# Kernel optimization log

Hardware: AMD Instinct MI355X
Metric: run time of the kernel (lower is better)

## Reference

```python
import jax, jax.numpy as jnp
import numpy as np

N_NODES = 50000
N_EDGES = 800000
IN_F, H_F, OUT_F = 512, 128, 64


def _graph_conv(x, W, b, src, dst, norm_src, norm_dst):
    # DGL GraphConv, norm='both': out = D_dst^-1/2 * A * (D_src^-1/2 * x) @ W + b
    # weight applied before aggregation (in_feats >= out_feats path) — math identical.
    h = (x * norm_src[:, None]) @ W                      # [N, out_f]
    agg = jax.ops.segment_sum(h[src], dst, num_segments=N_NODES)  # SpMM gather/scatter
    return agg * norm_dst[:, None] + b


def setup_inputs() -> dict:
    key = jax.random.key(0)
    ks = jax.random.split(key, 12)
    x = jax.random.normal(ks[0], (N_NODES, IN_F), dtype=jnp.float32)
    src = jax.random.randint(ks[1], (N_EDGES,), 0, N_NODES, dtype=jnp.int64)
    dst = jax.random.randint(ks[2], (N_EDGES,), 0, N_NODES, dtype=jnp.int64)

    def glorot(k, fan_in, fan_out):
        s = jnp.sqrt(6.0 / (fan_in + fan_out)).astype(jnp.float32)
        return jax.random.uniform(k, (fan_in, fan_out), jnp.float32, -s, s)

    return {
        'x': x, 'src': src, 'dst': dst,
        'W1': glorot(ks[3], IN_F, H_F), 'b1': jnp.zeros((H_F,), jnp.float32),
        'W2': glorot(ks[4], H_F, H_F), 'b2': jnp.zeros((H_F,), jnp.float32),
        'W3': glorot(ks[5], H_F, H_F), 'b3': jnp.zeros((H_F,), jnp.float32),
        'W4': glorot(ks[6], H_F, OUT_F), 'b4': jnp.zeros((OUT_F,), jnp.float32),
        'embedding_layer': 3,
    }


def reference(x, src, dst, W1, b1, W2, b2, W3, b3, W4, b4, embedding_layer):
    ones = jnp.ones((N_EDGES,), jnp.float32)
    out_deg = jnp.maximum(jax.ops.segment_sum(ones, src, num_segments=N_NODES), 1.0)
    in_deg = jnp.maximum(jax.ops.segment_sum(ones, dst, num_segments=N_NODES), 1.0)
    norm_src = jax.lax.rsqrt(out_deg)
    norm_dst = jax.lax.rsqrt(in_deg)

    h1 = jax.nn.relu(_graph_conv(x, W1, b1, src, dst, norm_src, norm_dst))
    h2 = jax.nn.relu(_graph_conv(h1, W2, b2, src, dst, norm_src, norm_dst))
    h3 = jax.nn.relu(_graph_conv(h2, W3, b3, src, dst, norm_src, norm_dst))
    h4 = _graph_conv(h3, W4, b4, src, dst, norm_src, norm_dst)

    hidden = [h1, h2, h3, h4][embedding_layer - 1]  # embedding_layer is a static int
    return (h4, hidden, x)
```

## Files before the change

### kernel.cpp

```cpp
#include <hip/hip_runtime.h>

#define N_NODES 50000
#define N_EDGES 800000
#define IN_F 512
#define H_F 128
#define OUT_F 64


__global__ void detect_kernel(const void* __restrict__ edges, int* __restrict__ flag) {
    if (threadIdx.x == 0 && blockIdx.x == 0) {
        const long long* p = (const long long*)edges;
        int is64 = 1;
        for (int k = 0; k < 256; k++) {
            long long v = p[k];
            if (v < 0 || v >= N_NODES) { is64 = 0; break; }
        }
        flag[0] = is64;
    }
}

__device__ __forceinline__ int edge_at(const void* __restrict__ p, int e, int is64) {
    return is64 ? (int)((const long long*)p)[e] : ((const int*)p)[e];
}

__global__ void count_kernel(const void* __restrict__ src, const void* __restrict__ dst,
                             int* __restrict__ cs, int* __restrict__ cd,
                             const int* __restrict__ flag) {
    int is64 = flag[0];
    int e = blockIdx.x * 256 + threadIdx.x;
    if (e < N_EDGES) {
        atomicAdd(&cs[edge_at(src, e, is64)], 1);
        atomicAdd(&cd[edge_at(dst, e, is64)], 1);
    }
}

__global__ void scan_kernel(const int* __restrict__ in, int* __restrict__ exc,
                            int* __restrict__ bsums, int n) {
    __shared__ int tmp[1024];
    int tid = threadIdx.x;
    int gid = blockIdx.x * 1024 + tid;
    int v = (gid < n) ? in[gid] : 0;
    tmp[tid] = v;
    __syncthreads();
    for (int off = 1; off < 1024; off <<= 1) {
        int t = (tid >= off) ? tmp[tid - off] : 0;
        __syncthreads();
        tmp[tid] += t;
        __syncthreads();
    }
    if (gid < n) exc[gid] = tmp[tid] - v;
    if (tid == 1023) bsums[blockIdx.x] = tmp[1023];
}

__global__ void finalize_kernel(const int* __restrict__ exc, const int* __restrict__ bexc,
                                int* __restrict__ rp, int* __restrict__ cur,
                                const int* __restrict__ cs, const int* __restrict__ cd,
                                float* __restrict__ ns, float* __restrict__ nd) {
    int i = blockIdx.x * 256 + threadIdx.x;
    if (i < N_NODES) {
        int v = exc[i] + bexc[i >> 10];
        rp[i] = v;
        cur[i] = v;
        if (i == 0) rp[N_NODES] = N_EDGES;
        ns[i] = 1.0f / sqrtf(fmaxf((float)cs[i], 1.0f));
        nd[i] = 1.0f / sqrtf(fmaxf((float)cd[i], 1.0f));
    }
}

__global__ void fill_kernel(const void* __restrict__ src, const void* __restrict__ dst,
                            int* __restrict__ cur, int* __restrict__ col,
                            const int* __restrict__ flag) {
    int is64 = flag[0];
    int e = blockIdx.x * 256 + threadIdx.x;
    if (e < N_EDGES) {
        int d = edge_at(dst, e, is64);
        int pos = atomicAdd(&cur[d], 1);
        col[pos] = edge_at(src, e, is64);
    }
}


__device__ __forceinline__ constexpr int swz(int f) { return f + (f >> 3); }

template <int N, int BM, bool COPY>
__global__ __launch_bounds__(256) void gemm_norm(const float* __restrict__ A, const float* __restrict__ W,
                                                 const float* __restrict__ norm, float* __restrict__ C,
                                                 int K, float* __restrict__ xc) {
    constexpr int TX = N / 8;
    constexpr int TY = 256 / TX;
    constexpr int RT = BM / TY;
    constexpr int NF4 = N / 4;
    constexpr int SA = BM + 4;
    constexpr int SW = (swz(NF4 - 1) + 2 + 3) / 4 * 4 * 4;

    __shared__ float Ast[32 * SA];
    __shared__ float Ws[32 * SW];

    const int t = threadIdx.x;
    const int tx = t % TX, ty = t / TX;
    const int m0 = blockIdx.x * BM;

    float acc[RT][8];
    #pragma unroll
    for (int i = 0; i < RT; i++)
        #pragma unroll
        for (int j = 0; j < 8; j++) acc[i][j] = 0.f;

    for (int k0 = 0; k0 < K; k0 += 32) {
        #pragma unroll
        for (int p = 0; p < BM * 32 / 4 / 256; p++) {
            int idx = t + p * 256;
            int r = idx >> 3;
            int c = (idx & 7) << 2;
            int row = m0 + r;
            float4 v = make_float4(0.f, 0.f, 0.f, 0.f);
            if (row < N_NODES) {
                v = *(const float4*)&A[(size_t)row * K + k0 + c];
                if (COPY) *(float4*)&xc[(size_t)row * K + k0 + c] = v;
            }
            Ast[(c + 0) * SA + r] = v.x;
            Ast[(c + 1) * SA + r] = v.y;
            Ast[(c + 2) * SA + r] = v.z;
            Ast[(c + 3) * SA + r] = v.w;
        }
        #pragma unroll
        for (int p = 0; p < 32 * NF4 / 256; p++) {
            int idx = t + p * 256;
            int r = idx / NF4;
            int f = idx % NF4;
            float4 wv = *(const float4*)&W[(size_t)(k0 + r) * N + f * 4];
            *(float4*)&Ws[r * SW + swz(f) * 4] = wv;
        }
        __syncthreads();
        #pragma unroll 8
        for (int kk = 0; kk < 32; kk++) {
            float a[RT], w[8];
            #pragma unroll
            for (int r4 = 0; r4 < RT / 4; r4++)
                *(float4*)&a[r4 * 4] = *(const float4*)&Ast[kk * SA + ty * RT + r4 * 4];
            int f0 = tx * 2;
            *(float4*)&w[0] = *(const float4*)&Ws[kk * SW + (f0 + (f0 >> 3)) * 4];
            *(float4*)&w[4] = *(const float4*)&Ws[kk * SW + (f0 + 1 + ((f0 + 1) >> 3)) * 4];
            #pragma unroll
            for (int i = 0; i < RT; i++)
                #pragma unroll
                for (int j = 0; j < 8; j++) acc[i][j] = fmaf(a[i], w[j], acc[i][j]);
        }
        __syncthreads();
    }
    #pragma unroll
    for (int i = 0; i < RT; i++) {
        int row = m0 + ty * RT + i;
        if (row < N_NODES) {
            float s = norm[row];
            float4 o0 = make_float4(acc[i][0] * s, acc[i][1] * s, acc[i][2] * s, acc[i][3] * s);
            float4 o1 = make_float4(acc[i][4] * s, acc[i][5] * s, acc[i][6] * s, acc[i][7] * s);
            *(float4*)&C[(size_t)row * N + tx * 8] = o0;
            *(float4*)&C[(size_t)row * N + tx * 8 + 4] = o1;
        }
    }
}


template <int FEAT, bool RELU, bool HID>
__global__ __launch_bounds__(256) void spmm_kernel(
        const float* __restrict__ h, const int* __restrict__ rp,
        const int* __restrict__ col, const float* __restrict__ nd,
        const float* __restrict__ bias, float* __restrict__ out,
        float* __restrict__ hid, const int* __restrict__ emb, int layer) {
    constexpr int VEC = FEAT / 64;
    int i = blockIdx.x * 4 + (threadIdx.x >> 6);
    i = __builtin_amdgcn_readfirstlane(i);
    if (i >= N_NODES) return;
    int lane = threadIdx.x & 63;
    int beg = rp[i], end = rp[i + 1];

    if (VEC == 2) {
        float ax = 0.f, ay = 0.f;
        int e = beg;
        for (; e + 4 <= end; e += 4) {
            int c0 = col[e], c1 = col[e + 1], c2 = col[e + 2], c3 = col[e + 3];
            float2 v0 = *(const float2*)&h[(size_t)c0 * FEAT + lane * 2];
            float2 v1 = *(const float2*)&h[(size_t)c1 * FEAT + lane * 2];
            float2 v2 = *(const float2*)&h[(size_t)c2 * FEAT + lane * 2];
            float2 v3 = *(const float2*)&h[(size_t)c3 * FEAT + lane * 2];
            ax += v0.x + v1.x + v2.x + v3.x;
            ay += v0.y + v1.y + v2.y + v3.y;
        }
        for (; e < end; e++) {
            float2 v = *(const float2*)&h[(size_t)col[e] * FEAT + lane * 2];
            ax += v.x; ay += v.y;
        }
        float s = nd[i];
        float2 b = *(const float2*)&bias[lane * 2];
        float vx = fmaf(ax, s, b.x), vy = fmaf(ay, s, b.y);
        if (RELU) { vx = fmaxf(vx, 0.f); vy = fmaxf(vy, 0.f); }
        float2 o = make_float2(vx, vy);
        *(float2*)&out[(size_t)i * FEAT + lane * 2] = o;
        if (HID) {
            if (emb[0] == layer) *(float2*)&hid[(size_t)i * FEAT + lane * 2] = o;
        }
    } else {
        float acc = 0.f;
        int e = beg;
        for (; e + 4 <= end; e += 4) {
            int c0 = col[e], c1 = col[e + 1], c2 = col[e + 2], c3 = col[e + 3];
            acc += h[(size_t)c0 * FEAT + lane];
            acc += h[(size_t)c1 * FEAT + lane];
            acc += h[(size_t)c2 * FEAT + lane];
            acc += h[(size_t)c3 * FEAT + lane];
        }
        for (; e < end; e++) acc += h[(size_t)col[e] * FEAT + lane];
        float v = fmaf(acc, nd[i], bias[lane]);
        if (RELU) v = fmaxf(v, 0.f);
        out[(size_t)i * FEAT + lane] = v;
        if (HID) {
            if (emb[0] == layer) hid[(size_t)i * FEAT + lane] = v;
        }
    }
}


extern "C" void kernel_launch(void* const* d_in, const int* in_sizes, int n_in,
                              void* d_out, int out_size, void* d_ws, size_t ws_size,
                              hipStream_t stream) {
    const float* x = (const float*)d_in[0];
    const void* src = d_in[1];
    const void* dst = d_in[2];
    const float* W1 = (const float*)d_in[3];  const float* b1 = (const float*)d_in[4];
    const float* W2 = (const float*)d_in[5];  const float* b2 = (const float*)d_in[6];
    const float* W3 = (const float*)d_in[7];  const float* b3 = (const float*)d_in[8];
    const float* W4 = (const float*)d_in[9];  const float* b4 = (const float*)d_in[10];
    const int* emb = (const int*)d_in[11];
    float* out = (float*)d_out;

    char* w = (char*)d_ws;
    int* cnt_src = (int*)w;  w += 51200 * 4;
    int* cnt_dst = (int*)w;  w += 51200 * 4;
    float* norm_src = (float*)w; w += 51200 * 4;
    float* norm_dst = (float*)w; w += 51200 * 4;
    int* exc = (int*)w;      w += 51200 * 4;
    int* bsums = (int*)w;    w += 1024 * 4;
    int* bexc = (int*)w;     w += 1024 * 4;
    int* bdummy = (int*)w;   w += 1024 * 4;
    int* dflag = (int*)w;    w += 1024 * 4;
    int* rp = (int*)w;       w += 51200 * 4;
    int* cur = (int*)w;      w += 51200 * 4;
    int* col = (int*)w;      w += 800768 * 4;
    float* gbuf = (float*)w; w += (size_t)6400000 * 4;
    float* hbuf = (float*)w; w += (size_t)6400000 * 4;

    hipMemsetAsync(cnt_src, 0, 2 * 51200 * 4, stream);
    detect_kernel<<<1, 64, 0, stream>>>(dst, dflag);
    count_kernel<<<3125, 256, 0, stream>>>(src, dst, cnt_src, cnt_dst, dflag);
    scan_kernel<<<49, 1024, 0, stream>>>(cnt_dst, exc, bsums, N_NODES);
    scan_kernel<<<1, 1024, 0, stream>>>(bsums, bexc, bdummy, 49);
    finalize_kernel<<<196, 256, 0, stream>>>(exc, bexc, rp, cur,
                                             cnt_src, cnt_dst, norm_src, norm_dst);
    fill_kernel<<<3125, 256, 0, stream>>>(src, dst, cur, col, dflag);

    const int GB = (N_NODES + 127) / 128;
    const int SB = (N_NODES + 3) / 4;
    float* hid = out + (size_t)N_NODES * OUT_F;
    float* xcopy = hid + (size_t)N_NODES * H_F;

    gemm_norm<128, 128, true><<<GB, 256, 0, stream>>>(x, W1, norm_src, gbuf, IN_F, xcopy);
    spmm_kernel<128, true, true><<<SB, 256, 0, stream>>>(gbuf, rp, col, norm_dst, b1, hbuf, hid, emb, 1);

    gemm_norm<128, 128, false><<<GB, 256, 0, stream>>>(hbuf, W2, norm_src, gbuf, H_F, nullptr);
    spmm_kernel<128, true, true><<<SB, 256, 0, stream>>>(gbuf, rp, col, norm_dst, b2, hbuf, hid, emb, 2);

    gemm_norm<128, 128, false><<<GB, 256, 0, stream>>>(hbuf, W3, norm_src, gbuf, H_F, nullptr);
    spmm_kernel<128, true, true><<<SB, 256, 0, stream>>>(gbuf, rp, col, norm_dst, b3, hbuf, hid, emb, 3);

    gemm_norm<64, 128, false><<<GB, 256, 0, stream>>>(hbuf, W4, norm_src, gbuf, H_F, nullptr);
    spmm_kernel<64, false, false><<<SB, 256, 0, stream>>>(gbuf, rp, col, norm_dst, b4, out, nullptr, nullptr, 0);
}
```

Before: 733.7 us.

## Register-prefetch GEMM tiles, shrink GEMM row tile, unroll SpMM gather by 8

The GEMM now loads the next K-tile into registers while computing the current one, and stores it to shared memory afterwards. This hides global load latency at the cost of an extra barrier and more registers. The 128-wide GEMMs use 64-row tiles for more blocks and occupancy, and the shared W padding is reduced. The SpMM gather loop is unrolled from 4 to 8 edges with tree-summed adds, so more loads are in flight per wave.

Measured after the change: 754.3 us. 1.03x slower.

```diff
diff --git a/kernel.cpp b/kernel.cpp
--- a/kernel.cpp
+++ b/kernel.cpp
@@ -91,7 +91,9 @@
     constexpr int RT = BM / TY;
     constexpr int NF4 = N / 4;
     constexpr int SA = BM + 4;
-    constexpr int SW = (swz(NF4 - 1) + 2 + 3) / 4 * 4 * 4;
+    constexpr int SW = (swz(NF4 - 1) + 1) * 4;
+    constexpr int APT = BM * 32 / 4 / 256;
+    constexpr int WPT = 32 * NF4 / 256;
 
     __shared__ float Ast[32 * SA];
     __shared__ float Ws[32 * SW];
@@ -99,39 +101,64 @@
     const int t = threadIdx.x;
     const int tx = t % TX, ty = t / TX;
     const int m0 = blockIdx.x * BM;
-
-    float acc[RT][8];
-    #pragma unroll
-    for (int i = 0; i < RT; i++)
-        #pragma unroll
-        for (int j = 0; j < 8; j++) acc[i][j] = 0.f;
-
-    for (int k0 = 0; k0 < K; k0 += 32) {
-        #pragma unroll
-        for (int p = 0; p < BM * 32 / 4 / 256; p++) {
+    const int KT = K / 32;
+
+    float4 abuf[APT], wbuf[WPT];
+
+    auto load_tile = [&](int k0) {
+        #pragma unroll
+        for (int p = 0; p < APT; p++) {
             int idx = t + p * 256;
             int r = idx >> 3;
             int c = (idx & 7) << 2;
             int row = m0 + r;
-            float4 v = make_float4(0.f, 0.f, 0.f, 0.f);
-            if (row < N_NODES) {
-                v = *(const float4*)&A[(size_t)row * K + k0 + c];
-                if (COPY) *(float4*)&xc[(size_t)row * K + k0 + c] = v;
-            }
-            Ast[(c + 0) * SA + r] = v.x;
-            Ast[(c + 1) * SA + r] = v.y;
-            Ast[(c + 2) * SA + r] = v.z;
-            Ast[(c + 3) * SA + r] = v.w;
-        }
-        #pragma unroll
-        for (int p = 0; p < 32 * NF4 / 256; p++) {
+            abuf[p] = make_float4(0.f, 0.f, 0.f, 0.f);
+            if (row < N_NODES) abuf[p] = *(const float4*)&A[(size_t)row * K + k0 + c];
+        }
+        #pragma unroll
+        for (int p = 0; p < WPT; p++) {
             int idx = t + p * 256;
             int r = idx / NF4;
             int f = idx % NF4;
-            float4 wv = *(const float4*)&W[(size_t)(k0 + r) * N + f * 4];
-            *(float4*)&Ws[r * SW + swz(f) * 4] = wv;
-        }
-        __syncthreads();
+            wbuf[p] = *(const float4*)&W[(size_t)(k0 + r) * N + f * 4];
+        }
+    };
+    auto store_tile = [&](int k0) {
+        #pragma unroll
+        for (int p = 0; p < APT; p++) {
+            int idx = t + p * 256;
+            int r = idx >> 3;
+            int c = (idx & 7) << 2;
+            Ast[(c + 0) * SA + r] = abuf[p].x;
+            Ast[(c + 1) * SA + r] = abuf[p].y;
+            Ast[(c + 2) * SA + r] = abuf[p].z;
+            Ast[(c + 3) * SA + r] = abuf[p].w;
+            if (COPY) {
+                int row = m0 + r;
+                if (row < N_NODES) *(float4*)&xc[(size_t)row * K + k0 + c] = abuf[p];
+            }
+        }
+        #pragma unroll
+        for (int p = 0; p < WPT; p++) {
+            int idx = t + p * 256;
+            int r = idx / NF4;
+            int f = idx % NF4;
+            *(float4*)&Ws[r * SW + swz(f) * 4] = wbuf[p];
+        }
+    };
+
+    float acc[RT][8];
+    #pragma unroll
+    for (int i = 0; i < RT; i++)
+        #pragma unroll
+        for (int j = 0; j < 8; j++) acc[i][j] = 0.f;
+
+    load_tile(0);
+    store_tile(0);
+    __syncthreads();
+
+    for (int kt = 0; kt < KT; kt++) {
+        if (kt + 1 < KT) load_tile((kt + 1) * 32);
         #pragma unroll 8
         for (int kk = 0; kk < 32; kk++) {
             float a[RT], w[8];
@@ -147,7 +174,12 @@
                 for (int j = 0; j < 8; j++) acc[i][j] = fmaf(a[i], w[j], acc[i][j]);
         }
         __syncthreads();
-    }
+        if (kt + 1 < KT) {
+            store_tile((kt + 1) * 32);
+            __syncthreads();
+        }
+    }
+
     #pragma unroll
     for (int i = 0; i < RT; i++) {
         int row = m0 + ty * RT + i;
@@ -168,24 +200,28 @@
         const int* __restrict__ col, const float* __restrict__ nd,
         const float* __restrict__ bias, float* __restrict__ out,
         float* __restrict__ hid, const int* __restrict__ emb, int layer) {
-    constexpr int VEC = FEAT / 64;
     int i = blockIdx.x * 4 + (threadIdx.x >> 6);
     i = __builtin_amdgcn_readfirstlane(i);
     if (i >= N_NODES) return;
     int lane = threadIdx.x & 63;
     int beg = rp[i], end = rp[i + 1];
 
-    if (VEC == 2) {
+    if constexpr (FEAT == 128) {
         float ax = 0.f, ay = 0.f;
         int e = beg;
-        for (; e + 4 <= end; e += 4) {
-            int c0 = col[e], c1 = col[e + 1], c2 = col[e + 2], c3 = col[e + 3];
+        for (; e + 8 <= end; e += 8) {
+            int c0 = col[e], c1 = col[e+1], c2 = col[e+2], c3 = col[e+3];
+            int c4 = col[e+4], c5 = col[e+5], c6 = col[e+6], c7 = col[e+7];
             float2 v0 = *(const float2*)&h[(size_t)c0 * FEAT + lane * 2];
             float2 v1 = *(const float2*)&h[(size_t)c1 * FEAT + lane * 2];
             float2 v2 = *(const float2*)&h[(size_t)c2 * FEAT + lane * 2];
             float2 v3 = *(const float2*)&h[(size_t)c3 * FEAT + lane * 2];
-            ax += v0.x + v1.x + v2.x + v3.x;
-            ay += v0.y + v1.y + v2.y + v3.y;
+            float2 v4 = *(const float2*)&h[(size_t)c4 * FEAT + lane * 2];
+            float2 v5 = *(const float2*)&h[(size_t)c5 * FEAT + lane * 2];
+            float2 v6 = *(const float2*)&h[(size_t)c6 * FEAT + lane * 2];
+            float2 v7 = *(const float2*)&h[(size_t)c7 * FEAT + lane * 2];
+            ax += (v0.x + v1.x) + (v2.x + v3.x) + ((v4.x + v5.x) + (v6.x + v7.x));
+            ay += (v0.y + v1.y) + (v2.y + v3.y) + ((v4.y + v5.y) + (v6.y + v7.y));
         }
         for (; e < end; e++) {
             float2 v = *(const float2*)&h[(size_t)col[e] * FEAT + lane * 2];
@@ -203,12 +239,18 @@
     } else {
         float acc = 0.f;
         int e = beg;
-        for (; e + 4 <= end; e += 4) {
-            int c0 = col[e], c1 = col[e + 1], c2 = col[e + 2], c3 = col[e + 3];
-            acc += h[(size_t)c0 * FEAT + lane];
-            acc += h[(size_t)c1 * FEAT + lane];
-            acc += h[(size_t)c2 * FEAT + lane];
-            acc += h[(size_t)c3 * FEAT + lane];
+        for (; e + 8 <= end; e += 8) {
+            int c0 = col[e], c1 = col[e+1], c2 = col[e+2], c3 = col[e+3];
+            int c4 = col[e+4], c5 = col[e+5], c6 = col[e+6], c7 = col[e+7];
+            float v0 = h[(size_t)c0 * FEAT + lane];
+            float v1 = h[(size_t)c1 * FEAT + lane];
+            float v2 = h[(size_t)c2 * FEAT + lane];
+            float v3 = h[(size_t)c3 * FEAT + lane];
+            float v4 = h[(size_t)c4 * FEAT + lane];
+            float v5 = h[(size_t)c5 * FEAT + lane];
+            float v6 = h[(size_t)c6 * FEAT + lane];
+            float v7 = h[(size_t)c7 * FEAT + lane];
+            acc += (v0 + v1) + (v2 + v3) + ((v4 + v5) + (v6 + v7));
         }
         for (; e < end; e++) acc += h[(size_t)col[e] * FEAT + lane];
         float v = fmaf(acc, nd[i], bias[lane]);
@@ -259,20 +301,21 @@
                                              cnt_src, cnt_dst, norm_src, norm_dst);
     fill_kernel<<<3125, 256, 0, stream>>>(src, dst, cur, col, dflag);
 
-    const int GB = (N_NODES + 127) / 128;
+    const int GB64 = (N_NODES + 63) / 64;
+    const int GB128 = (N_NODES + 127) / 128;
     const int SB = (N_NODES + 3) / 4;
     float* hid = out + (size_t)N_NODES * OUT_F;
     float* xcopy = hid + (size_t)N_NODES * H_F;
 
-    gemm_norm<128, 128, true><<<GB, 256, 0, stream>>>(x, W1, norm_src, gbuf, IN_F, xcopy);
+    gemm_norm<128, 64, true><<<GB64, 256, 0, stream>>>(x, W1, norm_src, gbuf, IN_F, xcopy);
     spmm_kernel<128, true, true><<<SB, 256, 0, stream>>>(gbuf, rp, col, norm_dst, b1, hbuf, hid, emb, 1);
 
-    gemm_norm<128, 128, false><<<GB, 256, 0, stream>>>(hbuf, W2, norm_src, gbuf, H_F, nullptr);
+    gemm_norm<128, 64, false><<<GB64, 256, 0, stream>>>(hbuf, W2, norm_src, gbuf, H_F, nullptr);
     spmm_kernel<128, true, true><<<SB, 256, 0, stream>>>(gbuf, rp, col, norm_dst, b2, hbuf, hid, emb, 2);
 
-    gemm_norm<128, 128, false><<<GB, 256, 0, stream>>>(hbuf, W3, norm_src, gbuf, H_F, nullptr);
+    gemm_norm<128, 64, false><<<GB64, 256, 0, stream>>>(hbuf, W3, norm_src, gbuf, H_F, nullptr);
     spmm_kernel<128, true, true><<<SB, 256, 0, stream>>>(gbuf, rp, col, norm_dst, b3, hbuf, hid, emb, 3);
 
-    gemm_norm<64, 128, false><<<GB, 256, 0, stream>>>(hbuf, W4, norm_src, gbuf, H_F, nullptr);
+    gemm_norm<64, 128, false><<<GB128, 256, 0, stream>>>(hbuf, W4, norm_src, gbuf, H_F, nullptr);
     spmm_kernel<64, false, false><<<SB, 256, 0, stream>>>(gbuf, rp, col, norm_dst, b4, out, nullptr, nullptr, 0);
 }
```
